# Kernel optimization log

Measured on AMD Instinct MI355X. Metric: run time of the kernel, lower is better.

The kernel has to match this reference:

```python
import jax, jax.numpy as jnp
import numpy as np
from jax import lax

B, S, D, H = 2, 2048, 1024, 16
DEPTH = D // H  # 64


def _leaky(x):
    # tf.keras.layers.ReLU(negative_slope=0.1)
    return jnp.where(x >= 0, x, 0.1 * x)


def _split_heads(x):
    # [B,S,D] -> [B,H,S,DEPTH]
    return x.reshape(B, S, H, DEPTH).transpose(0, 2, 1, 3)


def setup_inputs() -> dict:
    key = jax.random.key(0)
    ks = jax.random.split(key, 8)
    w = lambda k: 0.02 * jax.random.normal(k, (D, D), dtype=jnp.float32)
    return {
        "q": jax.random.normal(ks[0], (B, S, D), dtype=jnp.float32),
        "k": jax.random.normal(ks[1], (B, S, D), dtype=jnp.float32),
        "v": jax.random.normal(ks[2], (B, S, D), dtype=jnp.float32),
        "query_mask": jnp.ones((B, S, 1), dtype=jnp.float32),
        "key_mask": jnp.ones((B, S, 1), dtype=jnp.float32),
        "value_mask": jnp.ones((B, S, 1), dtype=jnp.float32),
        "Wq": w(ks[3]), "bq": 0.5 * jnp.ones((D,), dtype=jnp.float32),
        "Wk": w(ks[4]), "bk": 0.5 * jnp.ones((D,), dtype=jnp.float32),
        "Wv": w(ks[5]), "bv": jnp.zeros((D,), dtype=jnp.float32),
        "Wo": w(ks[6]), "bo": jnp.zeros((D,), dtype=jnp.float32),
    }


def _causal_linear_attn(qh, kh, vh):
    # qh,kh,vh: [B,H,S,DEPTH]. Sequential recurrence:
    #   S_t = S_{t-1} + k_t v_t^T ; z_t = z_{t-1} + k_t
    #   out_t = (q_t @ S_t) / (q_t . z_t)
    def step(carry, x):
        S_st, z = carry
        qi, ki, vi = x  # each [B,H,DEPTH]
        S_st = S_st + ki[..., :, None] * vi[..., None, :]  # [B,H,DEPTH,DEPTH]
        z = z + ki
        num = jnp.einsum('bhd,bhde->bhe', qi, S_st)
        den = jnp.einsum('bhd,bhd->bh', qi, z)
        return (S_st, z), num / den[..., None]

    init = (jnp.zeros((B, H, DEPTH, DEPTH), dtype=qh.dtype),
            jnp.zeros((B, H, DEPTH), dtype=qh.dtype))
    xs = (jnp.moveaxis(qh, 2, 0), jnp.moveaxis(kh, 2, 0), jnp.moveaxis(vh, 2, 0))
    _, out = lax.scan(step, init, xs)  # [S,B,H,DEPTH]
    return jnp.moveaxis(out, 0, 2)  # [B,H,S,DEPTH]


def reference(q, k, v, query_mask, key_mask, value_mask,
              Wq, bq, Wk, bk, Wv, bv, Wo, bo):
    q = (q * query_mask) @ Wq + bq
    k = (k * key_mask) @ Wk + bk
    v = (v * value_mask) @ Wv + bv
    q = _leaky(q)
    k = _leaky(k)
    qh, kh, vh = _split_heads(q), _split_heads(k), _split_heads(v)
    attn = _causal_linear_attn(qh, kh, vh)  # [B,H,S,DEPTH]
    concat = attn.transpose(0, 2, 1, 3).reshape(B, S, D)
    return concat @ Wo + bo
```

## Files before the change

kernel.cpp:

```cpp
#include <hip/hip_runtime.h>

#define Bx    2
#define Sx    2048
#define Dx    1024
#define Hx    16
#define NCx   (Sx/64)
#define BHx   (Bx*Hx)
#define Mx    (Bx*Sx)

typedef float    f4 __attribute__((ext_vector_type(4)));
typedef _Float16 h8 __attribute__((ext_vector_type(8)));
typedef _Float16 h4 __attribute__((ext_vector_type(4)));

__device__ __forceinline__ void gl2lds16(const _Float16* g, _Float16* l) {
  __builtin_amdgcn_global_load_lds(
      (const __attribute__((address_space(1))) void*)g,
      (__attribute__((address_space(3))) void*)l, 16, 0, 0);
}

__global__ __launch_bounds__(256) void convert_in(
    const float* __restrict__ q, const float* __restrict__ k,
    const float* __restrict__ v, const float* __restrict__ qm,
    const float* __restrict__ km, const float* __restrict__ vm,
    _Float16* __restrict__ qh, _Float16* __restrict__ kh,
    _Float16* __restrict__ vh)
{
  const int z = blockIdx.y;
  const float* x = (z == 0) ? q : (z == 1) ? k : v;
  const float* m = (z == 0) ? qm : (z == 1) ? km : vm;
  _Float16*    o = (z == 0) ? qh : (z == 1) ? kh : vh;
  const int i4 = blockIdx.x * 256 + threadIdx.x;
  const f4 vv = *(const f4*)(x + (size_t)i4 * 4);
  const float mf = m[i4 >> 8];
  h4 r;
  r[0] = (_Float16)(vv[0] * mf);
  r[1] = (_Float16)(vv[1] * mf);
  r[2] = (_Float16)(vv[2] * mf);
  r[3] = (_Float16)(vv[3] * mf);
  *(h4*)(o + (size_t)i4 * 4) = r;
}

__global__ __launch_bounds__(256) void convert_w(
    const float* __restrict__ W0, const float* __restrict__ W1,
    const float* __restrict__ W2, const float* __restrict__ W3,
    _Float16* __restrict__ T0, _Float16* __restrict__ T1,
    _Float16* __restrict__ T2, _Float16* __restrict__ T3)
{
  const float* W = (blockIdx.z == 0) ? W0 : (blockIdx.z == 1) ? W1 :
                   (blockIdx.z == 2) ? W2 : W3;
  _Float16* T = (blockIdx.z == 0) ? T0 : (blockIdx.z == 1) ? T1 :
                (blockIdx.z == 2) ? T2 : T3;
  __shared__ float Ws[64 * 68];
  const int tx = threadIdx.x & 15, ty = threadIdx.x >> 4;
  const int k0 = blockIdx.y * 64, n0 = blockIdx.x * 64;
#pragma unroll
  for (int i = 0; i < 4; i++) {
    const int r = ty + 16 * i;
    *(f4*)&Ws[r * 68 + tx * 4] = *(const f4*)&W[(size_t)(k0 + r) * Dx + n0 + tx * 4];
  }
  __syncthreads();
#pragma unroll
  for (int i = 0; i < 4; i++) {
    const int n = ty + 16 * i;
    h4 o;
#pragma unroll
    for (int j = 0; j < 4; j++) o[j] = (_Float16)Ws[(tx * 4 + j) * 68 + n];
    *(h4*)&T[(size_t)(n0 + n) * Dx + k0 + tx * 4] = o;
  }
}

struct GArgs {
  const _Float16* A; const _Float16* Bt; const float* bias;
  void* out; int leaky, half_out;
};

template<int BM, int BN, int WR, int WC>
__global__ __launch_bounds__(512, 4) void gemm_f16(GArgs g0, GArgs g1, GArgs g2)
{
  const GArgs g = (blockIdx.z == 0) ? g0 : (blockIdx.z == 1) ? g1 : g2;
  constexpr int FM = BM / WR / 16;
  constexpr int FN = BN / WC / 16;
  __shared__ _Float16 As[BM * 64];
  __shared__ _Float16 Bs[BN * 64];
  const int tid = threadIdx.x;
  const int m0 = blockIdx.y * BM, n0 = blockIdx.x * BN;
  const int lane = tid & 63, wave = tid >> 6;
  const int lm = lane & 15, qd = lane >> 4;
  const int wr = wave % WR, wc = wave / WR;
  const int wm0 = wr * (BM / WR), wn0 = wc * (BN / WC);
  const int srow = lane >> 3;
  const int sseg = (lane & 7) ^ srow;
  const _Float16* gA = g.A  + (size_t)(m0 + srow) * Dx + sseg * 8;
  const _Float16* gB = g.Bt + (size_t)(n0 + srow) * Dx + sseg * 8;

  f4 acc[FM][FN];
#pragma unroll
  for (int i = 0; i < FM; i++)
#pragma unroll
    for (int j = 0; j < FN; j++) { f4 z = {0.f, 0.f, 0.f, 0.f}; acc[i][j] = z; }

  for (int kt = 0; kt < Dx; kt += 64) {
    __syncthreads();
#pragma unroll
    for (int u = 0; u < BM / 64; u++) {
      const int t = wave * (BM / 64) + u;
      gl2lds16(gA + (size_t)(t * 8) * Dx + kt, &As[t * 512]);
    }
#pragma unroll
    for (int u = 0; u < BN / 64; u++) {
      const int t = wave * (BN / 64) + u;
      gl2lds16(gB + (size_t)(t * 8) * Dx + kt, &Bs[t * 512]);
    }
    __syncthreads();
#pragma unroll
    for (int kk = 0; kk < 2; kk++) {
      const int sp = ((kk * 4 + qd) ^ (lm & 7)) * 8;
      h8 af[FM];
#pragma unroll
      for (int i = 0; i < FM; i++)
        af[i] = *(const h8*)&As[(wm0 + i * 16 + lm) * 64 + sp];
#pragma unroll
      for (int j = 0; j < FN; j++) {
        const h8 bf = *(const h8*)&Bs[(wn0 + j * 16 + lm) * 64 + sp];
#pragma unroll
        for (int i = 0; i < FM; i++)
          acc[i][j] = __builtin_amdgcn_mfma_f32_16x16x32_f16(af[i], bf, acc[i][j], 0, 0, 0);
      }
    }
  }

#pragma unroll
  for (int j = 0; j < FN; j++) {
    const int n = n0 + wn0 + j * 16 + lm;
    const float bz = g.bias[n];
#pragma unroll
    for (int i = 0; i < FM; i++) {
      const int mb = m0 + wm0 + i * 16 + qd * 4;
#pragma unroll
      for (int r = 0; r < 4; r++) {
        float v = acc[i][j][r] + bz;
        if (g.leaky) v = (v >= 0.f) ? v : 0.1f * v;
        if (g.half_out) ((_Float16*)g.out)[(size_t)(mb + r) * Dx + n] = (_Float16)v;
        else            ((float*)g.out)[(size_t)(mb + r) * Dx + n] = v;
      }
    }
  }
}

__global__ __launch_bounds__(256) void chunkkv_mfma(
    const _Float16* __restrict__ kp, const _Float16* __restrict__ vp,
    _Float16* __restrict__ ckvh, float* __restrict__ cz)
{
  __shared__ _Float16 Kt[64 * 64];
  __shared__ _Float16 Vt[64 * 64];
  const int blk = blockIdx.x;
  const int c = blk & (NCx - 1);
  const int bh = blk / NCx;
  const int b = bh / Hx, h = bh % Hx;
  const int tid = threadIdx.x;
  const size_t rowbase = ((size_t)(b * Sx + c * 64)) * Dx + h * 64;

#pragma unroll
  for (int p = 0; p < 2; p++) {
    const int f = tid + 256 * p;
    const int s = f >> 3, g8 = f & 7;
    const h8 hk = *(const h8*)&kp[rowbase + (size_t)s * Dx + g8 * 8];
    const h8 hv = *(const h8*)&vp[rowbase + (size_t)s * Dx + g8 * 8];
#pragma unroll
    for (int i = 0; i < 8; i++) {
      const int r = g8 * 8 + i;
      const int a = r * 64 + (((s >> 3) ^ (r & 7)) * 8) + (s & 7);
      Kt[a] = hk[i];
      Vt[a] = hv[i];
    }
  }
  __syncthreads();

  const int lane = tid & 63, w = tid >> 6;
  const int lm = lane & 15, qd = lane >> 4;
  const int x7 = lm & 7;

  h8 av[2];
#pragma unroll
  for (int kk = 0; kk < 2; kk++)
    av[kk] = *(const h8*)&Vt[(w * 16 + lm) * 64 + (((kk << 2) + qd) ^ x7) * 8];

#pragma unroll
  for (int dt = 0; dt < 4; dt++) {
    f4 acc = {0.f, 0.f, 0.f, 0.f};
#pragma unroll
    for (int kk = 0; kk < 2; kk++) {
      const h8 bf = *(const h8*)&Kt[(dt * 16 + lm) * 64 + (((kk << 2) + qd) ^ x7) * 8];
      acc = __builtin_amdgcn_mfma_f32_16x16x32_f16(av[kk], bf, acc, 0, 0, 0);
    }
#pragma unroll
    for (int r = 0; r < 4; r++) {
      const int e = w * 16 + qd * 4 + r;
      ckvh[(size_t)blk * 4096 + e * 64 + dt * 16 + lm] = (_Float16)acc[r];
    }
  }

  {
    const int d = tid >> 2, fr = tid & 3;
    float dp = 0.f;
#pragma unroll
    for (int j = 0; j < 2; j++) {
      const h8 kv = *(const h8*)&Kt[d * 64 + (fr * 2 + j) * 8];
#pragma unroll
      for (int i = 0; i < 8; i++) dp += (float)kv[i];
    }
    dp += __shfl_xor(dp, 1);
    dp += __shfl_xor(dp, 2);
    if (fr == 0) cz[(size_t)blk * 64 + d] = dp;
  }
}

__global__ __launch_bounds__(256) void prefix_kernel(
    _Float16* __restrict__ ckvh, float* __restrict__ cz)
{
  const int gid = blockIdx.x * 256 + threadIdx.x;
  const int bh = gid >> 12, el = gid & 4095;
  float acc = 0.f;
  for (int c = 0; c < NCx; c++) {
    const size_t idx = ((size_t)(bh * NCx + c) << 12) + el;
    const float v = (float)ckvh[idx];
    ckvh[idx] = (_Float16)acc;
    acc += v;
  }
  if (gid < BHx * 64) {
    const int zbh = gid >> 6, d = gid & 63;
    float az = 0.f;
    for (int c = 0; c < NCx; c++) {
      const size_t zi = (size_t)(zbh * NCx + c) * 64 + d;
      const float v = cz[zi];
      cz[zi] = az;
      az += v;
    }
  }
}

__global__ __launch_bounds__(256) void attn_mfma(
    const _Float16* __restrict__ qp, const _Float16* __restrict__ kp,
    const _Float16* __restrict__ vp, const _Float16* __restrict__ ckvh,
    const float* __restrict__ cz, _Float16* __restrict__ concat)
{
  __shared__ _Float16 Qs[64 * 64];
  __shared__ _Float16 Ks[64 * 64];
  __shared__ _Float16 Vt[64 * 64];
  __shared__ _Float16 Sh[64 * 64];
  __shared__ float zs[64];
  __shared__ float den[64];
  const int blk = blockIdx.x;
  const int c = blk & (NCx - 1);
  const int bh = blk / NCx;
  const int b = bh / Hx, h = bh % Hx;
  const int tid = threadIdx.x;
  const size_t rowbase = ((size_t)(b * Sx + c * 64)) * Dx + h * 64;

#pragma unroll
  for (int p = 0; p < 2; p++) {
    const int f = tid + 256 * p;
    const int r = f >> 3, sg = f & 7;
    const int ph = (sg ^ (r & 7)) * 8;
    *(h8*)&Qs[r * 64 + ph] = *(const h8*)&qp[rowbase + (size_t)r * Dx + sg * 8];
    *(h8*)&Ks[r * 64 + ph] = *(const h8*)&kp[rowbase + (size_t)r * Dx + sg * 8];
    *(h8*)&Sh[r * 64 + ph] = *(const h8*)&ckvh[(size_t)blk * 4096 + r * 64 + sg * 8];
  }
#pragma unroll
  for (int p = 0; p < 2; p++) {
    const int f = tid + 256 * p;
    const int s = f >> 3, g8 = f & 7;
    const h8 hv = *(const h8*)&vp[rowbase + (size_t)s * Dx + g8 * 8];
#pragma unroll
    for (int i = 0; i < 8; i++) {
      const int e = g8 * 8 + i;
      Vt[e * 64 + (((s >> 3) ^ (e & 7)) * 8) + (s & 7)] = hv[i];
    }
  }
  if (tid < 64) zs[tid] = cz[(size_t)blk * 64 + tid];
  __syncthreads();

  const int lane = tid & 63, w = tid >> 6;
  const int lm = lane & 15, qd = lane >> 4;
  const int x7 = lm & 7;

  h8 aq[2];
#pragma unroll
  for (int kk = 0; kk < 2; kk++)
    aq[kk] = *(const h8*)&Qs[(w * 16 + lm) * 64 + (((kk << 2) + qd) ^ x7) * 8];

  f4 pc[4];
#pragma unroll
  for (int st = 0; st < 4; st++) {
    f4 z4 = {0.f, 0.f, 0.f, 0.f}; pc[st] = z4;
#pragma unroll
    for (int kk = 0; kk < 2; kk++) {
      const h8 bf = *(const h8*)&Ks[(st * 16 + lm) * 64 + (((kk << 2) + qd) ^ x7) * 8];
      pc[st] = __builtin_amdgcn_mfma_f32_16x16x32_f16(aq[kk], bf, pc[st], 0, 0, 0);
    }
  }
  float rsum[4] = {0.f, 0.f, 0.f, 0.f};
#pragma unroll
  for (int st = 0; st < 4; st++) {
    const int s = st * 16 + lm;
#pragma unroll
    for (int r = 0; r < 4; r++) {
      const int t = w * 16 + qd * 4 + r;
      float v = pc[st][r];
      v = (s <= t) ? v : 0.f;
      pc[st][r] = v;
      rsum[r] += v;
    }
  }
#pragma unroll
  for (int r = 0; r < 4; r++) {
    rsum[r] += __shfl_xor(rsum[r], 1);
    rsum[r] += __shfl_xor(rsum[r], 2);
    rsum[r] += __shfl_xor(rsum[r], 4);
    rsum[r] += __shfl_xor(rsum[r], 8);
  }
  {
    const int t = tid >> 2, fr = tid & 3;
    float dp = 0.f;
#pragma unroll
    for (int j = 0; j < 2; j++) {
      const int sg = fr * 2 + j;
      const h8 qv = *(const h8*)&Qs[t * 64 + (sg ^ (t & 7)) * 8];
#pragma unroll
      for (int i = 0; i < 8; i++) dp += (float)qv[i] * zs[sg * 8 + i];
    }
    dp += __shfl_xor(dp, 1);
    dp += __shfl_xor(dp, 2);
    if (fr == 0) den[t] = dp;
  }
  __syncthreads();

  _Float16* Pa = Ks;
#pragma unroll
  for (int st = 0; st < 4; st++) {
#pragma unroll
    for (int r = 0; r < 4; r++) {
      const int row = w * 16 + qd * 4 + r;
      Pa[row * 64 + (((st * 2 + (lm >> 3)) ^ (row & 7)) * 8) + (lm & 7)] =
          (_Float16)pc[st][r];
    }
  }
  if (lm == 0) {
#pragma unroll
    for (int r = 0; r < 4; r++) den[w * 16 + qd * 4 + r] += rsum[r];
  }
  __syncthreads();

  h8 ap[2];
#pragma unroll
  for (int kk = 0; kk < 2; kk++)
    ap[kk] = *(const h8*)&Pa[(w * 16 + lm) * 64 + (((kk << 2) + qd) ^ x7) * 8];

  f4 acc[4];
#pragma unroll
  for (int et = 0; et < 4; et++) {
    f4 z4 = {0.f, 0.f, 0.f, 0.f}; acc[et] = z4;
#pragma unroll
    for (int kk = 0; kk < 2; kk++) {
      const h8 bv = *(const h8*)&Vt[(et * 16 + lm) * 64 + (((kk << 2) + qd) ^ x7) * 8];
      acc[et] = __builtin_amdgcn_mfma_f32_16x16x32_f16(ap[kk], bv, acc[et], 0, 0, 0);
    }
#pragma unroll
    for (int kk = 0; kk < 2; kk++) {
      const h8 bs = *(const h8*)&Sh[(et * 16 + lm) * 64 + (((kk << 2) + qd) ^ x7) * 8];
      acc[et] = __builtin_amdgcn_mfma_f32_16x16x32_f16(aq[kk], bs, acc[et], 0, 0, 0);
    }
  }

#pragma unroll
  for (int r = 0; r < 4; r++) {
    const int row = w * 16 + qd * 4 + r;
    const float inv = 1.f / den[row];
    _Float16* orow = &concat[((size_t)(b * Sx + c * 64 + row)) * Dx + h * 64];
#pragma unroll
    for (int et = 0; et < 4; et++)
      orow[et * 16 + lm] = (_Float16)(acc[et][r] * inv);
  }
}

extern "C" void kernel_launch(void* const* d_in, const int* in_sizes, int n_in,
                              void* d_out, int out_size, void* d_ws, size_t ws_size,
                              hipStream_t stream)
{
  const float* q  = (const float*)d_in[0];
  const float* k  = (const float*)d_in[1];
  const float* v  = (const float*)d_in[2];
  const float* qm = (const float*)d_in[3];
  const float* km = (const float*)d_in[4];
  const float* vm = (const float*)d_in[5];
  const float* Wq = (const float*)d_in[6];
  const float* bq = (const float*)d_in[7];
  const float* Wk = (const float*)d_in[8];
  const float* bk = (const float*)d_in[9];
  const float* Wv = (const float*)d_in[10];
  const float* bv = (const float*)d_in[11];
  const float* Wo = (const float*)d_in[12];
  const float* bo = (const float*)d_in[13];
  float* out = (float*)d_out;

  char* ws = (char*)d_ws;
  _Float16* qh  = (_Float16*)(ws);
  _Float16* kh  = (_Float16*)(ws + 8388608);
  _Float16* vh  = (_Float16*)(ws + 16777216);
  _Float16* Wtq = (_Float16*)(ws + 25165824);
  _Float16* Wtk = (_Float16*)(ws + 27262976);
  _Float16* Wtv = (_Float16*)(ws + 29360128);
  _Float16* Wto = (_Float16*)(ws + 31457280);
  _Float16* qp  = (_Float16*)(ws + 33554432);
  _Float16* kp  = (_Float16*)(ws + 41943040);
  _Float16* vp  = (_Float16*)(ws + 50331648);
  float*    cz  = (float*)   (ws + 58720256);
  _Float16* ckvh   = qh;
  _Float16* concat = kh;

  convert_in<<<dim3(4096, 3), 256, 0, stream>>>(q, k, v, qm, km, vm, qh, kh, vh);
  convert_w<<<dim3(16, 16, 4), 256, 0, stream>>>(Wq, Wk, Wv, Wo, Wtq, Wtk, Wtv, Wto);

  GArgs gq = { qh, Wtq, bq, qp, 1, 1 };
  GArgs gk = { kh, Wtk, bk, kp, 1, 1 };
  GArgs gv = { vh, Wtv, bv, vp, 0, 1 };
  gemm_f16<128, 128, 2, 4><<<dim3(Dx / 128, Mx / 128, 3), 512, 0, stream>>>(gq, gk, gv);

  chunkkv_mfma<<<BHx * NCx, 256, 0, stream>>>(kp, vp, ckvh, cz);
  prefix_kernel<<<512, 256, 0, stream>>>(ckvh, cz);
  attn_mfma<<<BHx * NCx, 256, 0, stream>>>(qp, kp, vp, ckvh, cz, concat);

  GArgs go = { concat, Wto, bo, out, 0, 0 };
  gemm_f16<64, 128, 2, 4><<<dim3(Dx / 128, Mx / 64, 1), 512, 0, stream>>>(go, go, go);
}
```

Measured before the change: 208.6 us.

## Double-buffer GEMM LDS tiles and fold QKV selection into grid x dimension

```diff
diff --git a/kernel.cpp b/kernel.cpp
--- a/kernel.cpp
+++ b/kernel.cpp
@@ -77,13 +77,15 @@
 template<int BM, int BN, int WR, int WC>
 __global__ __launch_bounds__(512, 4) void gemm_f16(GArgs g0, GArgs g1, GArgs g2)
 {
-  const GArgs g = (blockIdx.z == 0) ? g0 : (blockIdx.z == 1) ? g1 : g2;
+  const int nglob = blockIdx.x * BN;
+  const GArgs g = (nglob < 1024) ? g0 : (nglob < 2048) ? g1 : g2;
+  const int n0 = nglob & 1023;
   constexpr int FM = BM / WR / 16;
   constexpr int FN = BN / WC / 16;
-  __shared__ _Float16 As[BM * 64];
-  __shared__ _Float16 Bs[BN * 64];
+  __shared__ _Float16 As[2][BM * 64];
+  __shared__ _Float16 Bs[2][BN * 64];
   const int tid = threadIdx.x;
-  const int m0 = blockIdx.y * BM, n0 = blockIdx.x * BN;
+  const int m0 = blockIdx.y * BM;
   const int lane = tid & 63, wave = tid >> 6;
   const int lm = lane & 15, qd = lane >> 4;
   const int wr = wave % WR, wc = wave / WR;
@@ -99,40 +101,55 @@
 #pragma unroll
     for (int j = 0; j < FN; j++) { f4 z = {0.f, 0.f, 0.f, 0.f}; acc[i][j] = z; }
 
-  for (int kt = 0; kt < Dx; kt += 64) {
-    __syncthreads();
-#pragma unroll
-    for (int u = 0; u < BM / 64; u++) {
-      const int t = wave * (BM / 64) + u;
-      gl2lds16(gA + (size_t)(t * 8) * Dx + kt, &As[t * 512]);
-    }
-#pragma unroll
-    for (int u = 0; u < BN / 64; u++) {
-      const int t = wave * (BN / 64) + u;
-      gl2lds16(gB + (size_t)(t * 8) * Dx + kt, &Bs[t * 512]);
-    }
-    __syncthreads();
+#pragma unroll
+  for (int u = 0; u < BM / 64; u++) {
+    const int t = wave * (BM / 64) + u;
+    gl2lds16(gA + (size_t)(t * 8) * Dx, &As[0][t * 512]);
+  }
+#pragma unroll
+  for (int u = 0; u < BN / 64; u++) {
+    const int t = wave * (BN / 64) + u;
+    gl2lds16(gB + (size_t)(t * 8) * Dx, &Bs[0][t * 512]);
+  }
+  __syncthreads();
+
+  for (int it = 0; it < Dx / 64; it++) {
+    const int buf = it & 1;
+    if (it < Dx / 64 - 1) {
+      const int kt = (it + 1) * 64;
+#pragma unroll
+      for (int u = 0; u < BM / 64; u++) {
+        const int t = wave * (BM / 64) + u;
+        gl2lds16(gA + (size_t)(t * 8) * Dx + kt, &As[buf ^ 1][t * 512]);
+      }
+#pragma unroll
+      for (int u = 0; u < BN / 64; u++) {
+        const int t = wave * (BN / 64) + u;
+        gl2lds16(gB + (size_t)(t * 8) * Dx + kt, &Bs[buf ^ 1][t * 512]);
+      }
+    }
 #pragma unroll
     for (int kk = 0; kk < 2; kk++) {
       const int sp = ((kk * 4 + qd) ^ (lm & 7)) * 8;
       h8 af[FM];
 #pragma unroll
       for (int i = 0; i < FM; i++)
-        af[i] = *(const h8*)&As[(wm0 + i * 16 + lm) * 64 + sp];
+        af[i] = *(const h8*)&As[buf][(wm0 + i * 16 + lm) * 64 + sp];
 #pragma unroll
       for (int j = 0; j < FN; j++) {
-        const h8 bf = *(const h8*)&Bs[(wn0 + j * 16 + lm) * 64 + sp];
+        const h8 bf = *(const h8*)&Bs[buf][(wn0 + j * 16 + lm) * 64 + sp];
 #pragma unroll
         for (int i = 0; i < FM; i++)
           acc[i][j] = __builtin_amdgcn_mfma_f32_16x16x32_f16(af[i], bf, acc[i][j], 0, 0, 0);
       }
     }
+    __syncthreads();
   }
 
 #pragma unroll
   for (int j = 0; j < FN; j++) {
-    const int n = n0 + wn0 + j * 16 + lm;
-    const float bz = g.bias[n];
+    const int n = wn0 + j * 16 + lm;
+    const float bz = g.bias[n0 + n];
 #pragma unroll
     for (int i = 0; i < FM; i++) {
       const int mb = m0 + wm0 + i * 16 + qd * 4;
@@ -140,8 +157,8 @@
       for (int r = 0; r < 4; r++) {
         float v = acc[i][j][r] + bz;
         if (g.leaky) v = (v >= 0.f) ? v : 0.1f * v;
-        if (g.half_out) ((_Float16*)g.out)[(size_t)(mb + r) * Dx + n] = (_Float16)v;
-        else            ((float*)g.out)[(size_t)(mb + r) * Dx + n] = v;
+        if (g.half_out) ((_Float16*)g.out)[(size_t)(mb + r) * Dx + n0 + n] = (_Float16)v;
+        else            ((float*)g.out)[(size_t)(mb + r) * Dx + n0 + n] = v;
       }
     }
   }
@@ -424,12 +441,12 @@
   GArgs gq = { qh, Wtq, bq, qp, 1, 1 };
   GArgs gk = { kh, Wtk, bk, kp, 1, 1 };
   GArgs gv = { vh, Wtv, bv, vp, 0, 1 };
-  gemm_f16<128, 128, 2, 4><<<dim3(Dx / 128, Mx / 128, 3), 512, 0, stream>>>(gq, gk, gv);
+  gemm_f16<128, 128, 2, 4><<<dim3(3072 / 128, Mx / 128), 512, 0, stream>>>(gq, gk, gv);
 
   chunkkv_mfma<<<BHx * NCx, 256, 0, stream>>>(kp, vp, ckvh, cz);
   prefix_kernel<<<512, 256, 0, stream>>>(ckvh, cz);
   attn_mfma<<<BHx * NCx, 256, 0, stream>>>(qp, kp, vp, ckvh, cz, concat);
 
   GArgs go = { concat, Wto, bo, out, 0, 0 };
-  gemm_f16<64, 128, 2, 4><<<dim3(Dx / 128, Mx / 64, 1), 512, 0, stream>>>(go, go, go);
-}
+  gemm_f16<128, 128, 2, 4><<<dim3(Dx / 128, Mx / 128), 512, 0, stream>>>(go, go, go);
+}
```

New measurement: 215.2 us. 1.03x slower.
